# Kernel tuning notes

Hardware: AMD Instinct MI355X
Metric: run time of the kernel (lower is better)

## Reference

```python
import jax, jax.numpy as jnp
import numpy as np

N = 50000   # nodes
E = 800000  # edges (no self loops; conv adds them)
F = 64      # in_channels == out_channels
P = 6       # pos dim (pos_nn MLP input = 6)
H = 64      # hidden width of pos_nn / attn_nn


def _mlp(x, W1, b1, W2, b2):
    # PyG MLP([a, 64, b], norm=None, plain_last=False): ReLU after both layers
    return jax.nn.relu(jax.nn.relu(x @ W1 + b1) @ W2 + b2)


def setup_inputs() -> dict:
    key = jax.random.key(0)
    ks = jax.random.split(key, 16)

    def w(k, shape, fan_in):
        return jax.random.normal(k, shape, jnp.float32) / np.sqrt(fan_in)

    src = jax.random.randint(ks[0], (E,), 0, N)
    dst = jax.random.randint(ks[1], (E,), 0, N)
    src = jnp.where(src == dst, (src + 1) % N, src)  # no pre-existing self loops
    edge_index = jnp.stack([src, dst]).astype(jnp.int32)

    return dict(
        x=jax.random.normal(ks[2], (N, F), jnp.float32),
        pos=jax.random.normal(ks[3], (N, P), jnp.float32),
        edge_index=edge_index,
        W_in=w(ks[4], (F, F), F), b_in=jnp.zeros((F,), jnp.float32),
        W_out=w(ks[5], (F, F), F), b_out=jnp.zeros((F,), jnp.float32),
        W_lin=w(ks[6], (F, F), F),   # conv value proj, bias=False
        W_src=w(ks[7], (F, F), F),   # lin_src, bias=False
        W_dst=w(ks[8], (F, F), F),   # lin_dst, bias=False
        Wp1=w(ks[9], (P, H), P), bp1=jnp.zeros((H,), jnp.float32),
        Wp2=w(ks[10], (H, F), H), bp2=jnp.zeros((F,), jnp.float32),
        Wa1=w(ks[11], (F, H), F), ba1=jnp.zeros((H,), jnp.float32),
        Wa2=w(ks[12], (H, F), H), ba2=jnp.zeros((F,), jnp.float32),
    )


def reference(x, pos, edge_index, W_in, b_in, W_out, b_out, W_lin, W_src, W_dst,
              Wp1, bp1, Wp2, bp2, Wa1, ba1, Wa2, ba2):
    residual = jax.lax.stop_gradient(x)  # residual = x.clone().detach()
    h = jax.nn.relu(x @ W_in + b_in)

    # PointTransformerConv
    a_src = h @ W_src
    a_dst = h @ W_dst
    v = h @ W_lin

    loop = jnp.arange(N, dtype=edge_index.dtype)  # add_self_loops=True
    src = jnp.concatenate([edge_index[0], loop])
    dst = jnp.concatenate([edge_index[1], loop])

    delta = _mlp(pos[dst] - pos[src], Wp1, bp1, Wp2, bp2)        # pos_nn(pos_i - pos_j)
    alpha = _mlp(a_dst[dst] - a_src[src] + delta, Wa1, ba1, Wa2, ba2)

    # scatter-softmax over destination neighborhoods (per channel)
    m = jax.ops.segment_max(alpha, dst, num_segments=N)
    e = jnp.exp(alpha - m[dst])
    s = jax.ops.segment_sum(e, dst, num_segments=N)
    wgt = e / (s[dst] + 1e-16)

    msg = wgt * (v[src] + delta)
    out = jax.ops.segment_sum(msg, dst, num_segments=N)

    out = jax.nn.relu(out @ W_out + b_out)
    return out + residual
```

## Files before the change

kernel.cpp:

```cpp
#include <hip/hip_runtime.h>

#define NN 50000
#define NE 800000
#define ETOT (NE + NN)
#define NB ((NN + 255) / 256)
#define SCATB ((NE + 255) / 256)
#define NODEB ((NN / 16 + 3) / 4)

typedef _Float16 f16;
typedef _Float16 v8h __attribute__((ext_vector_type(8)));
typedef float v4f __attribute__((ext_vector_type(4)));

__device__ __forceinline__ float bcast(float v, int lane) {
  return __int_as_float(__builtin_amdgcn_readlane(__float_as_int(v), lane));
}

__device__ __forceinline__ int fr_off(int kb, int nb, int q, int p) {
  return (((nb * 2 + kb) * 4 + q) * 16 + p) * 8;
}


__global__ __launch_bounds__(256) void k_setup(
    const float* __restrict__ W_in, const float* __restrict__ W_src,
    const float* __restrict__ W_dst, const float* __restrict__ W_lin,
    const float* __restrict__ W_out, const float* __restrict__ Wp2,
    const float* __restrict__ Wa1, const float* __restrict__ Wa2,
    const float* __restrict__ Wp1, f16* __restrict__ FR,
    const int* __restrict__ edst, int* __restrict__ deg) {
  const int t = blockIdx.x * 256 + threadIdx.x;
  if (t < NE) atomicAdd(&deg[edst[t]], 1);
  if (t < 8 * 4096) {
    const float* Ws[8] = {W_in, W_src, W_dst, W_lin, W_out, Wp2, Wa1, Wa2};
    const int m = t >> 12, idx = t & 4095;
    const int i = idx & 7, p = (idx >> 3) & 15, q = (idx >> 7) & 3;
    const int kb = (idx >> 9) & 1, nb = (idx >> 10) & 3;
    FR[t] = (f16)Ws[m][(kb * 32 + q * 8 + i) * 64 + nb * 16 + p];
  } else if (t < 8 * 4096 + 2048) {
    const int idx = t - 8 * 4096;
    const int i = idx & 7, p = (idx >> 3) & 15, q = (idx >> 7) & 3, nb = idx >> 9;
    const int k = q * 8 + i;
    FR[t] = (k < 6) ? (f16)Wp1[k * 64 + nb * 16 + p] : (f16)0.f;
  }
}


__global__ __launch_bounds__(256) void k_scan1(const int* __restrict__ deg,
                                               int* __restrict__ bsum) {
  __shared__ int ws[4];
  const int t = threadIdx.x, b = blockIdx.x;
  const int i = b * 256 + t;
  int s = (i < NN) ? (deg[i] + 1) : 0;
#pragma unroll
  for (int d = 1; d < 64; d <<= 1) s += __shfl_xor(s, d, 64);
  if ((t & 63) == 0) ws[t >> 6] = s;
  __syncthreads();
  if (t == 0) bsum[b] = ws[0] + ws[1] + ws[2] + ws[3];
}

__global__ __launch_bounds__(256) void k_scan3(
    const int* __restrict__ deg, const int* __restrict__ bsum,
    int* __restrict__ offsets, int* __restrict__ ssrc, int* __restrict__ cursor) {
  __shared__ int r1[4], r2[4], ws[4], wpre[4];
  __shared__ int bbase;
  const int t = threadIdx.x, b = blockIdx.x, lane = t & 63, w = t >> 6;
  int bs = (t < NB) ? bsum[t] : 0;
  int pr = (t < b) ? bs : 0;
#pragma unroll
  for (int d = 1; d < 64; d <<= 1) {
    pr += __shfl_xor(pr, d, 64);
    bs += __shfl_xor(bs, d, 64);
  }
  if (lane == 0) { r1[w] = pr; r2[w] = bs; }
  __syncthreads();
  if (t == 0) {
    bbase = r1[0] + r1[1] + r1[2] + r1[3];
    if (b == 0) offsets[NN] = r2[0] + r2[1] + r2[2] + r2[3];
  }
  __syncthreads();
  const int i = b * 256 + t;
  int v = (i < NN) ? (deg[i] + 1) : 0;
  int x = v;
#pragma unroll
  for (int d = 1; d < 64; d <<= 1) {
    int y = __shfl_up(x, d, 64);
    if (lane >= d) x += y;
  }
  if (lane == 63) ws[w] = x;
  __syncthreads();
  if (t == 0) {
    int c = 0;
#pragma unroll
    for (int j = 0; j < 4; ++j) { wpre[j] = c; c += ws[j]; }
  }
  __syncthreads();
  if (i < NN) {
    const int off = bbase + wpre[w] + x - v;
    offsets[i] = off;
    ssrc[off] = i;
    cursor[i] = off + 1;
  }
}


__global__ __launch_bounds__(256, 2) void k_scnode(
    const int* __restrict__ esrc, const int* __restrict__ edst,
    int* __restrict__ cursor, int* __restrict__ ssrc,
    const float* __restrict__ x, const float* __restrict__ pos,
    const float* __restrict__ b_in, const f16* __restrict__ FR,
    f16* __restrict__ adsth, f16* __restrict__ vh,
    f16* __restrict__ asrch, f16* __restrict__ Qh) {
  __shared__ f16 lds[4][16 * 72];
  const int b = blockIdx.x;
  if (b < SCATB) {
    const int e = b * 256 + threadIdx.x;
    if (e < NE) {
      int pp = atomicAdd(&cursor[edst[e]], 1);
      ssrc[pp] = esrc[e];
    }
    return;
  }
  const int lane = threadIdx.x & 63, w = threadIdx.x >> 6;
  const int q = lane >> 4, p = lane & 15;
  const int base = ((b - SCATB) * 4 + w) * 16;
  if (base >= NN) return;
  const f16* FWin = FR;
  const f16* FWsrc = FR + 1 * 4096;
  const f16* FWdst = FR + 2 * 4096;
  const f16* FWlin = FR + 3 * 4096;
  const f16* FWp1 = FR + 8 * 4096;

  v8h xa[2];
#pragma unroll
  for (int kb = 0; kb < 2; ++kb) {
    const float4 f0 = *(const float4*)(x + (base + p) * 64 + kb * 32 + q * 8);
    const float4 f1 = *(const float4*)(x + (base + p) * 64 + kb * 32 + q * 8 + 4);
    v8h a;
    a[0] = (f16)f0.x; a[1] = (f16)f0.y; a[2] = (f16)f0.z; a[3] = (f16)f0.w;
    a[4] = (f16)f1.x; a[5] = (f16)f1.y; a[6] = (f16)f1.z; a[7] = (f16)f1.w;
    xa[kb] = a;
  }
#pragma unroll
  for (int nb = 0; nb < 4; ++nb) {
    v4f c = {0.f, 0.f, 0.f, 0.f};
    c = __builtin_amdgcn_mfma_f32_16x16x32_f16(xa[0], *(const v8h*)&FWin[fr_off(0, nb, q, p)], c, 0, 0, 0);
    c = __builtin_amdgcn_mfma_f32_16x16x32_f16(xa[1], *(const v8h*)&FWin[fr_off(1, nb, q, p)], c, 0, 0, 0);
    const float bi = b_in[p + 16 * nb];
#pragma unroll
    for (int r = 0; r < 4; ++r)
      lds[w][(q * 4 + r) * 72 + p + 16 * nb] = (f16)fmaxf(c[r] + bi, 0.f);
  }
  v8h hA[2];
#pragma unroll
  for (int kb = 0; kb < 2; ++kb)
    hA[kb] = *(const v8h*)&lds[w][p * 72 + kb * 32 + q * 8];

#pragma unroll
  for (int nb = 0; nb < 4; ++nb) {
    v4f c = {0.f, 0.f, 0.f, 0.f};
    c = __builtin_amdgcn_mfma_f32_16x16x32_f16(hA[0], *(const v8h*)&FWsrc[fr_off(0, nb, q, p)], c, 0, 0, 0);
    c = __builtin_amdgcn_mfma_f32_16x16x32_f16(hA[1], *(const v8h*)&FWsrc[fr_off(1, nb, q, p)], c, 0, 0, 0);
#pragma unroll
    for (int r = 0; r < 4; ++r)
      asrch[(base + q * 4 + r) * 64 + p + 16 * nb] = (f16)c[r];
  }
#pragma unroll
  for (int nb = 0; nb < 4; ++nb) {
    v4f c = {0.f, 0.f, 0.f, 0.f};
    c = __builtin_amdgcn_mfma_f32_16x16x32_f16(hA[0], *(const v8h*)&FWdst[fr_off(0, nb, q, p)], c, 0, 0, 0);
    c = __builtin_amdgcn_mfma_f32_16x16x32_f16(hA[1], *(const v8h*)&FWdst[fr_off(1, nb, q, p)], c, 0, 0, 0);
#pragma unroll
    for (int r = 0; r < 4; ++r)
      adsth[(base + q * 4 + r) * 64 + p + 16 * nb] = (f16)c[r];
  }
#pragma unroll
  for (int nb = 0; nb < 4; ++nb) {
    v4f c = {0.f, 0.f, 0.f, 0.f};
    c = __builtin_amdgcn_mfma_f32_16x16x32_f16(hA[0], *(const v8h*)&FWlin[fr_off(0, nb, q, p)], c, 0, 0, 0);
    c = __builtin_amdgcn_mfma_f32_16x16x32_f16(hA[1], *(const v8h*)&FWlin[fr_off(1, nb, q, p)], c, 0, 0, 0);
#pragma unroll
    for (int r = 0; r < 4; ++r)
      vh[(base + q * 4 + r) * 64 + p + 16 * nb] = (f16)c[r];
  }
  v8h pa;
#pragma unroll
  for (int i = 0; i < 8; ++i) {
    const int k = q * 8 + i;
    pa[i] = (k < 6) ? (f16)pos[(base + p) * 6 + k] : (f16)0.f;
  }
#pragma unroll
  for (int nb = 0; nb < 4; ++nb) {
    const v8h bb = *(const v8h*)&FWp1[(((nb * 4 + q) * 16) + p) * 8];
    v4f c = {0.f, 0.f, 0.f, 0.f};
    c = __builtin_amdgcn_mfma_f32_16x16x32_f16(pa, bb, c, 0, 0, 0);
#pragma unroll
    for (int r = 0; r < 4; ++r)
      Qh[(base + q * 4 + r) * 64 + p + 16 * nb] = (f16)c[r];
  }
}


__global__ __launch_bounds__(512, 6) void k_conv(
    const f16* __restrict__ Qh, const float* __restrict__ bp1,
    const f16* __restrict__ FRconv,
    const float* __restrict__ bp2, const float* __restrict__ ba1,
    const float* __restrict__ ba2,
    const f16* __restrict__ asrch, const f16* __restrict__ adsth,
    const f16* __restrict__ vh,
    const int* __restrict__ offsets, const int* __restrict__ ssrc,
    const float* __restrict__ W_out, const float* __restrict__ b_out,
    const float* __restrict__ x, float* __restrict__ out) {
  __shared__ f16 wfr[12288];
  __shared__ f16 tbuf[8][16 * 72];
  __shared__ f16 stashQ[8][64];
  __shared__ f16 stashA[8][64];
  __shared__ float bias[192];
  const int t = threadIdx.x;
#pragma unroll
  for (int it = 0; it < 3; ++it)
    *(uint4*)&wfr[(it * 512 + t) * 8] = *(const uint4*)&FRconv[(it * 512 + t) * 8];
  if (t < 192) bias[t] = (t < 64) ? bp2[t] : (t < 128 ? ba1[t - 64] : ba2[t - 128]);

  const int lane = t & 63, w = t >> 6;
  const int q = lane >> 4, p = lane & 15;
  const int n = blockIdx.x * 8 + w;

  stashQ[w][lane] = (f16)((float)Qh[n * 64 + lane] + bp1[lane]);
  stashA[w][lane] = adsth[n * 64 + lane];
  __syncthreads();

  const int e0 = __builtin_amdgcn_readfirstlane(offsets[n]);
  const int e1 = __builtin_amdgcn_readfirstlane(offsets[n + 1]);
  const int cnt = e1 - e0;

  float s_[4], ac_[4];
#pragma unroll
  for (int nb = 0; nb < 4; ++nb) { s_[nb] = 0.f; ac_[nb] = 0.f; }

  for (int cb = 0; cb < cnt; cb += 16) {
    const int jA = ssrc[e0 + min(cb + p, cnt - 1)];
    v8h qj[2], aj[2], vA[2];
#pragma unroll
    for (int kb = 0; kb < 2; ++kb) {
      qj[kb] = *(const v8h*)(Qh + jA * 64 + kb * 32 + q * 8);
      aj[kb] = *(const v8h*)(asrch + jA * 64 + kb * 32 + q * 8);
      vA[kb] = *(const v8h*)(vh + jA * 64 + kb * 32 + q * 8);
    }
    v8h uA[2];
#pragma unroll
    for (int kb = 0; kb < 2; ++kb) {
      const v8h qi = *(const v8h*)&stashQ[w][kb * 32 + q * 8];
      v8h a;
#pragma unroll
      for (int i = 0; i < 8; ++i) {
        const f16 d = qi[i] - qj[kb][i];
        a[i] = d > (f16)0 ? d : (f16)0;
      }
      uA[kb] = a;
    }
    unsigned z0;
    asm volatile("v_mov_b32 %0, 0" : "=v"(z0));
    v8h dc0, dc1;
#pragma unroll
    for (int nb = 0; nb < 4; ++nb) {
      v4f c = {0.f, 0.f, 0.f, 0.f};
      c = __builtin_amdgcn_mfma_f32_16x16x32_f16(uA[0], *(const v8h*)&wfr[z0 + fr_off(0, nb, q, p)], c, 0, 0, 0);
      c = __builtin_amdgcn_mfma_f32_16x16x32_f16(uA[1], *(const v8h*)&wfr[z0 + fr_off(1, nb, q, p)], c, 0, 0, 0);
      const float bp2c = bias[p + 16 * nb];
#pragma unroll
      for (int r = 0; r < 4; ++r) {
        const f16 dh = (f16)fmaxf(c[r] + bp2c, 0.f);
        tbuf[w][(q * 4 + r) * 72 + p + 16 * nb] = dh;
        const int idx = nb * 4 + r;
        if (idx < 8) dc0[idx] = dh; else dc1[idx - 8] = dh;
      }
    }
#pragma unroll
    for (int kb = 0; kb < 2; ++kb) {
      const v8h adc = *(const v8h*)&stashA[w][kb * 32 + q * 8];
      const v8h dj = *(const v8h*)&tbuf[w][p * 72 + kb * 32 + q * 8];
      uA[kb] = (adc - aj[kb]) + dj;
    }
    unsigned z1;
    asm volatile("v_mov_b32 %0, 4096" : "=v"(z1));
#pragma unroll
    for (int nb = 0; nb < 4; ++nb) {
      v4f c = {0.f, 0.f, 0.f, 0.f};
      c = __builtin_amdgcn_mfma_f32_16x16x32_f16(uA[0], *(const v8h*)&wfr[z1 + fr_off(0, nb, q, p)], c, 0, 0, 0);
      c = __builtin_amdgcn_mfma_f32_16x16x32_f16(uA[1], *(const v8h*)&wfr[z1 + fr_off(1, nb, q, p)], c, 0, 0, 0);
      const float ba1c = bias[64 + p + 16 * nb];
#pragma unroll
      for (int r = 0; r < 4; ++r)
        tbuf[w][(q * 4 + r) * 72 + p + 16 * nb] = (f16)fmaxf(c[r] + ba1c, 0.f);
    }
#pragma unroll
    for (int kb = 0; kb < 2; ++kb)
      uA[kb] = *(const v8h*)&tbuf[w][p * 72 + kb * 32 + q * 8];
#pragma unroll
    for (int kb = 0; kb < 2; ++kb)
      *(v8h*)&tbuf[w][p * 72 + kb * 32 + q * 8] = vA[kb];
    unsigned z2;
    asm volatile("v_mov_b32 %0, 8192" : "=v"(z2));
#pragma unroll
    for (int nb = 0; nb < 4; ++nb) {
      v4f c = {0.f, 0.f, 0.f, 0.f};
      c = __builtin_amdgcn_mfma_f32_16x16x32_f16(uA[0], *(const v8h*)&wfr[z2 + fr_off(0, nb, q, p)], c, 0, 0, 0);
      c = __builtin_amdgcn_mfma_f32_16x16x32_f16(uA[1], *(const v8h*)&wfr[z2 + fr_off(1, nb, q, p)], c, 0, 0, 0);
      const float ba2c = bias[128 + p + 16 * nb];
#pragma unroll
      for (int r = 0; r < 4; ++r) {
        const bool ok = (cb + q * 4 + r) < cnt;
        const float al = ok ? fmaxf(c[r] + ba2c, 0.f) : -3.0e38f;
        const float wv = __expf(al);
        const float vj = (float)tbuf[w][(q * 4 + r) * 72 + p + 16 * nb];
        const int idx = nb * 4 + r;
        const float dC = (float)((idx < 8) ? dc0[idx] : dc1[idx - 8]);
        s_[nb] += wv;
        ac_[nb] = fmaf(wv, vj + dC, ac_[nb]);
      }
    }
  }
#pragma unroll
  for (int st = 16; st <= 32; st <<= 1) {
#pragma unroll
    for (int nb = 0; nb < 4; ++nb) {
      s_[nb] += __shfl_xor(s_[nb], st, 64);
      ac_[nb] += __shfl_xor(ac_[nb], st, 64);
    }
  }
  const float o = ac_[q] / (s_[q] + 1e-16f);
  float a0 = b_out[lane], a1 = 0.f, a2 = 0.f, a3 = 0.f;
#pragma unroll
  for (int k = 0; k < 64; k += 4) {
    a0 = fmaf(bcast(o, k + 0), W_out[(k + 0) * 64 + lane], a0);
    a1 = fmaf(bcast(o, k + 1), W_out[(k + 1) * 64 + lane], a1);
    a2 = fmaf(bcast(o, k + 2), W_out[(k + 2) * 64 + lane], a2);
    a3 = fmaf(bcast(o, k + 3), W_out[(k + 3) * 64 + lane], a3);
  }
  out[n * 64 + lane] = fmaxf((a0 + a1) + (a2 + a3), 0.f) + x[n * 64 + lane];
}


extern "C" void kernel_launch(void* const* d_in, const int* in_sizes, int n_in,
                              void* d_out, int out_size, void* d_ws, size_t ws_size,
                              hipStream_t stream) {
  const float* x     = (const float*)d_in[0];
  const float* pos   = (const float*)d_in[1];
  const int*   ei    = (const int*)d_in[2];
  const float* W_in  = (const float*)d_in[3];
  const float* b_in  = (const float*)d_in[4];
  const float* W_out = (const float*)d_in[5];
  const float* b_out = (const float*)d_in[6];
  const float* W_lin = (const float*)d_in[7];
  const float* W_src = (const float*)d_in[8];
  const float* W_dst = (const float*)d_in[9];
  const float* Wp1   = (const float*)d_in[10];
  const float* bp1   = (const float*)d_in[11];
  const float* Wp2   = (const float*)d_in[12];
  const float* bp2   = (const float*)d_in[13];
  const float* Wa1   = (const float*)d_in[14];
  const float* ba1   = (const float*)d_in[15];
  const float* Wa2   = (const float*)d_in[16];
  const float* ba2   = (const float*)d_in[17];

  f16*  Qh     = (f16*)d_ws;
  f16*  asrch  = Qh + NN * 64;
  f16*  adsth  = asrch + NN * 64;
  f16*  vh     = adsth + NN * 64;
  f16*  FR     = vh + NN * 64;
  int*  deg    = (int*)(FR + 8 * 4096 + 2048);
  int* offsets = deg + NN;
  int* cursor  = offsets + NN + 1;
  int* bsum    = cursor + NN;
  int* ssrc    = bsum + NB;

  const int* esrc = ei;
  const int* edst = ei + NE;

  hipMemsetAsync(deg, 0, NN * sizeof(int), stream);
  k_setup<<<(NE + 255) / 256, 256, 0, stream>>>(
      W_in, W_src, W_dst, W_lin, W_out, Wp2, Wa1, Wa2, Wp1, FR, edst, deg);
  k_scan1<<<NB, 256, 0, stream>>>(deg, bsum);
  k_scan3<<<NB, 256, 0, stream>>>(deg, bsum, offsets, ssrc, cursor);
  k_scnode<<<SCATB + NODEB, 256, 0, stream>>>(esrc, edst, cursor, ssrc,
                                              x, pos, b_in, FR,
                                              adsth, vh, asrch, Qh);
  k_conv<<<NN / 8, 512, 0, stream>>>(Qh, bp1, FR + 5 * 4096, bp2, ba1, ba2,
                                     asrch, adsth, vh, offsets, ssrc,
                                     W_out, b_out, x, (float*)d_out);
}
```

Before: 307.1 us.

## Fuse scan kernels and bucket nodes by degree for balanced conv waves

Merges the two-pass block-sum scan into one kernel in which every block recomputes the prefix of earlier blocks directly from deg. It also sorts nodes into three degree buckets (<=16, <=32, larger) with atomics, and the conv kernel reads its node from these ordered lists. Wavefronts in a block then have similar edge-loop trip counts. The costs are a redundant O(N) read per scan block, atomic contention on three counters, an extra indirection per node in conv, and scattered memory access to node data.

```diff
diff --git a/kernel.cpp b/kernel.cpp
--- a/kernel.cpp
+++ b/kernel.cpp
@@ -44,33 +44,27 @@
 }
 
 
-__global__ __launch_bounds__(256) void k_scan1(const int* __restrict__ deg,
-                                               int* __restrict__ bsum) {
-  __shared__ int ws[4];
-  const int t = threadIdx.x, b = blockIdx.x;
-  const int i = b * 256 + t;
-  int s = (i < NN) ? (deg[i] + 1) : 0;
-#pragma unroll
-  for (int d = 1; d < 64; d <<= 1) s += __shfl_xor(s, d, 64);
-  if ((t & 63) == 0) ws[t >> 6] = s;
-  __syncthreads();
-  if (t == 0) bsum[b] = ws[0] + ws[1] + ws[2] + ws[3];
-}
-
-__global__ __launch_bounds__(256) void k_scan3(
-    const int* __restrict__ deg, const int* __restrict__ bsum,
-    int* __restrict__ offsets, int* __restrict__ ssrc, int* __restrict__ cursor) {
+__global__ __launch_bounds__(256) void k_scan(
+    const int* __restrict__ deg, int* __restrict__ offsets,
+    int* __restrict__ ssrc, int* __restrict__ cursor,
+    int* __restrict__ bcnt, int* __restrict__ ord0,
+    int* __restrict__ ord1, int* __restrict__ ord2) {
   __shared__ int r1[4], r2[4], ws[4], wpre[4];
   __shared__ int bbase;
   const int t = threadIdx.x, b = blockIdx.x, lane = t & 63, w = t >> 6;
-  int bs = (t < NB) ? bsum[t] : 0;
-  int pr = (t < b) ? bs : 0;
+  int pr = 0, tot = 0;
+  for (int k = 0; k < NB; ++k) {
+    const int idx = k * 256 + t;
+    const int v = (idx < NN) ? (deg[idx] + 1) : 0;
+    tot += v;
+    if (k < b) pr += v;
+  }
 #pragma unroll
   for (int d = 1; d < 64; d <<= 1) {
     pr += __shfl_xor(pr, d, 64);
-    bs += __shfl_xor(bs, d, 64);
-  }
-  if (lane == 0) { r1[w] = pr; r2[w] = bs; }
+    tot += __shfl_xor(tot, d, 64);
+  }
+  if (lane == 0) { r1[w] = pr; r2[w] = tot; }
   __syncthreads();
   if (t == 0) {
     bbase = r1[0] + r1[1] + r1[2] + r1[3];
@@ -98,6 +92,9 @@
     offsets[i] = off;
     ssrc[off] = i;
     cursor[i] = off + 1;
+    const int bk = (v <= 16) ? 0 : (v <= 32 ? 1 : 2);
+    const int pos = atomicAdd(&bcnt[bk], 1);
+    (bk == 0 ? ord0 : bk == 1 ? ord1 : ord2)[pos] = i;
   }
 }
 
@@ -207,6 +204,8 @@
     const f16* __restrict__ asrch, const f16* __restrict__ adsth,
     const f16* __restrict__ vh,
     const int* __restrict__ offsets, const int* __restrict__ ssrc,
+    const int* __restrict__ bcnt, const int* __restrict__ ord0,
+    const int* __restrict__ ord1, const int* __restrict__ ord2,
     const float* __restrict__ W_out, const float* __restrict__ b_out,
     const float* __restrict__ x, float* __restrict__ out) {
   __shared__ f16 wfr[12288];
@@ -222,7 +221,9 @@
 
   const int lane = t & 63, w = t >> 6;
   const int q = lane >> 4, p = lane & 15;
-  const int n = blockIdx.x * 8 + w;
+  const int g = blockIdx.x * 8 + w;
+  const int c0 = bcnt[0], c01 = c0 + bcnt[1];
+  const int n = (g < c0) ? ord0[g] : (g < c01) ? ord1[g - c0] : ord2[g - c01];
 
   stashQ[w][lane] = (f16)((float)Qh[n * 64 + lane] + bp1[lane]);
   stashA[w][lane] = adsth[n * 64 + lane];
@@ -368,23 +369,26 @@
   f16*  vh     = adsth + NN * 64;
   f16*  FR     = vh + NN * 64;
   int*  deg    = (int*)(FR + 8 * 4096 + 2048);
-  int* offsets = deg + NN;
+  int*  bcnt   = deg + NN;
+  int* offsets = bcnt + 4;
   int* cursor  = offsets + NN + 1;
-  int* bsum    = cursor + NN;
-  int* ssrc    = bsum + NB;
+  int* ord0    = cursor + NN;
+  int* ord1    = ord0 + NN;
+  int* ord2    = ord1 + NN;
+  int* ssrc    = ord2 + NN;
 
   const int* esrc = ei;
   const int* edst = ei + NE;
 
-  hipMemsetAsync(deg, 0, NN * sizeof(int), stream);
+  hipMemsetAsync(deg, 0, (NN + 4) * sizeof(int), stream);
   k_setup<<<(NE + 255) / 256, 256, 0, stream>>>(
       W_in, W_src, W_dst, W_lin, W_out, Wp2, Wa1, Wa2, Wp1, FR, edst, deg);
-  k_scan1<<<NB, 256, 0, stream>>>(deg, bsum);
-  k_scan3<<<NB, 256, 0, stream>>>(deg, bsum, offsets, ssrc, cursor);
+  k_scan<<<NB, 256, 0, stream>>>(deg, offsets, ssrc, cursor, bcnt, ord0, ord1, ord2);
   k_scnode<<<SCATB + NODEB, 256, 0, stream>>>(esrc, edst, cursor, ssrc,
                                               x, pos, b_in, FR,
                                               adsth, vh, asrch, Qh);
   k_conv<<<NN / 8, 512, 0, stream>>>(Qh, bp1, FR + 5 * 4096, bp2, ba1, ba2,
                                      asrch, adsth, vh, offsets, ssrc,
+                                     bcnt, ord0, ord1, ord2,
                                      W_out, b_out, x, (float*)d_out);
 }
```

Measured after the change: 718.9 us. 2.34x slower.
